# Kernel tuning notes

Hardware: AMD Instinct MI355X
Metric: run time of the kernel (lower is better)

Reference implementation:

```python
import jax, jax.numpy as jnp
import numpy as np

N = 100000      # nodes
D = 128         # input feature dim
K = 8           # propagation hops (concat K+1 blocks)
HID = 512
OUT = 32
E = 1600000     # edges (avg degree 16)
BN_EPS = 1e-5
DEG_EPS = 1e-8


def setup_inputs() -> dict:
    key = jax.random.key(0)
    ks = jax.random.split(key, 8)
    feature = jax.random.normal(ks[0], (N, D), dtype=jnp.float32)
    coor = jax.random.uniform(ks[1], (N, 2), dtype=jnp.float32)
    edge_index = jax.random.randint(ks[2], (2, E), 0, N, dtype=jnp.int32)
    theta = jnp.array(1.0, dtype=jnp.float32)  # Gaussian bandwidth param
    fan1 = D * (K + 1)
    W1 = jax.random.normal(ks[3], (HID, fan1), dtype=jnp.float32) * (1.0 / np.sqrt(fan1))
    b1 = jnp.zeros((HID,), dtype=jnp.float32)
    gamma = jnp.ones((HID,), dtype=jnp.float32)
    beta = jnp.zeros((HID,), dtype=jnp.float32)
    W2 = jax.random.normal(ks[4], (OUT, HID), dtype=jnp.float32) * (1.0 / np.sqrt(HID))
    b2 = jnp.zeros((OUT,), dtype=jnp.float32)
    return {"feature": feature, "coor": coor, "theta": theta,
            "W1": W1, "b1": b1, "gamma": gamma, "beta": beta,
            "W2": W2, "b2": b2, "edge_index": edge_index, "m": 1}


def reference(feature, coor, theta, W1, b1, gamma, beta, W2, b2, edge_index, m):
    row, col = edge_index[0], edge_index[1]  # dst, src
    # Gaussian kernel edge weights from coordinate distances (gather on coor)
    diff = coor[row] - coor[col]                       # [E, 2]
    dist2 = jnp.sum(diff * diff, axis=-1)              # [E]
    w = jnp.exp(-dist2 * theta / m)                    # [E]
    # degree (row) normalization via scatter-add
    deg = jax.ops.segment_sum(w, row, num_segments=N)  # [N]
    norm = w / (deg[row] + DEG_EPS)                    # [E]
    # K sequential propagations, concat with input (-> N x D*(K+1))
    xs = [feature]
    x = feature
    for _ in range(K):
        msgs = x[col] * norm[:, None]                  # [E, D] gather + weight
        x = jax.ops.segment_sum(msgs, row, num_segments=N)  # [N, D] scatter
        xs.append(x)
    h = jnp.concatenate(xs, axis=-1)                   # [N, D*(K+1)]
    # MLP head: fc1 -> leaky_relu(0.2) -> BatchNorm1d (batch stats) -> fc2
    h = jax.nn.leaky_relu(h @ W1.T + b1, negative_slope=0.2)
    mu = jnp.mean(h, axis=0)
    var = jnp.var(h, axis=0)
    h = (h - mu) * jax.lax.rsqrt(var + BN_EPS) * gamma + beta
    # dropout omitted (deterministic/eval reference)
    return h @ W2.T + b2
```

## Files before the change

kernel.cpp:

```cpp
#include <hip/hip_runtime.h>
#include <hip/hip_bf16.h>
#include <cstdint>
#include <cstddef>

#define NNODES 100000
#define DFEAT 128
#define KHOP 8
#define FAN1 1152
#define HIDN 512
#define OUTD 32
#define NEDGE 1600000
#define BN_EPS 1e-5f
#define DEG_EPS 1e-8f
#define FIXSCALE 67108864.0f

using short8 = __attribute__((ext_vector_type(8))) short;
using f32x4  = __attribute__((ext_vector_type(4))) float;

__device__ __forceinline__ float bf16lo(uint32_t u) { return __uint_as_float(u << 16); }
__device__ __forceinline__ float bf16hi(uint32_t u) { return __uint_as_float(u & 0xffff0000u); }
__device__ __forceinline__ float bf16s(short x) {
    return __uint_as_float(((uint32_t)(uint16_t)x) << 16);
}
__device__ __forceinline__ uint32_t packbf(float a, float b) {
    uint32_t lo = __bfloat16_as_ushort(__float2bfloat16(a));
    uint32_t hi = __bfloat16_as_ushort(__float2bfloat16(b));
    return lo | (hi << 16);
}

__device__ __forceinline__ void gload16(const void* g, void* l) {
    __builtin_amdgcn_global_load_lds(
        (const __attribute__((address_space(1))) uint32_t*)g,
        (__attribute__((address_space(3))) uint32_t*)l, 16, 0, 0);
}

struct Blk3 { const __hip_bfloat16* p[3]; };

__global__ __launch_bounds__(256) void edge_kernel(
    const int* __restrict__ ei, const float* __restrict__ coor,
    const float* __restrict__ theta, const int* __restrict__ mm,
    unsigned long long* __restrict__ packed, unsigned short* __restrict__ rank)
{
    int e = blockIdx.x * 256 + threadIdx.x;
    if (e >= NEDGE) return;
    float tom = theta[0] / (float)mm[0];
    int r = ei[e], c = ei[NEDGE + e];
    float2 pr = *(const float2*)(coor + 2*(size_t)r);
    float2 pc = *(const float2*)(coor + 2*(size_t)c);
    float dx = pr.x - pc.x, dy = pr.y - pc.y;
    float w = expf(-(dx*dx + dy*dy) * tom);
    unsigned long long enc = (1ULL << 48)
        | (unsigned long long)(unsigned int)__float2uint_rn(w * FIXSCALE);
    unsigned long long old = atomicAdd(&packed[r], enc);
    rank[e] = (unsigned short)(old >> 48);
}

__global__ __launch_bounds__(1024) void scan_local(
    const unsigned long long* __restrict__ packed, int* __restrict__ row_ptr,
    int* __restrict__ bsum, int n)
{
    __shared__ int wsum[16];
    int b = blockIdx.x, tid = threadIdx.x;
    int i = b * 1024 + tid;
    int lane = tid & 63, wv = tid >> 6;
    int v = (i < n) ? (int)(packed[i] >> 48) : 0;
    #pragma unroll
    for (int off = 1; off < 64; off <<= 1) {
        int t = __shfl_up(v, off, 64);
        if (lane >= off) v += t;
    }
    if (lane == 63) wsum[wv] = v;
    __syncthreads();
    if (tid < 16) {
        int t = wsum[tid];
        #pragma unroll
        for (int off = 1; off < 16; off <<= 1) {
            int u = __shfl_up(t, off, 64);
            if (tid >= off) t += u;
        }
        wsum[tid] = t;
    }
    __syncthreads();
    int incl = v + ((wv == 0) ? 0 : wsum[wv - 1]);
    if (i < n) row_ptr[i + 1] = incl;
    if (tid == 0) bsum[b] = wsum[15];
}

__global__ __launch_bounds__(128) void scan_carry(int* __restrict__ bsum, int n)
{
    __shared__ int ws[2];
    int tid = threadIdx.x, lane = tid & 63, wv = tid >> 6;
    int v = (tid < n) ? bsum[tid] : 0;
    int incl = v;
    #pragma unroll
    for (int off = 1; off < 64; off <<= 1) {
        int t = __shfl_up(incl, off, 64);
        if (lane >= off) incl += t;
    }
    if (lane == 63) ws[wv] = incl;
    __syncthreads();
    int excl = incl - v + ((wv == 0) ? 0 : ws[0]);
    if (tid < n) bsum[tid] = excl;
}

__global__ __launch_bounds__(256) void scan_add(
    const int* __restrict__ bsum, int* __restrict__ row_ptr, int n)
{
    int i = blockIdx.x * 256 + threadIdx.x;
    if (i == 0) row_ptr[0] = 0;
    if (i < n) row_ptr[i + 1] += bsum[i >> 10];
}

__global__ __launch_bounds__(256) void fill_kernel(
    const int* __restrict__ ei, const float* __restrict__ coor,
    const float* __restrict__ theta, const int* __restrict__ mm,
    const unsigned long long* __restrict__ packed,
    const unsigned short* __restrict__ rank, const int* __restrict__ row_ptr,
    uint2* __restrict__ edat)
{
    int e = blockIdx.x * 256 + threadIdx.x;
    if (e >= NEDGE) return;
    float tom = theta[0] / (float)mm[0];
    int r = ei[e], c = ei[NEDGE + e];
    float2 pr = *(const float2*)(coor + 2*(size_t)r);
    float2 pc = *(const float2*)(coor + 2*(size_t)c);
    float dx = pr.x - pc.x, dy = pr.y - pc.y;
    float w = expf(-(dx*dx + dy*dy) * tom);
    float deg = (float)(double)(packed[r] & 0xFFFFFFFFFFFFULL) * (1.0f / FIXSCALE);
    int pos = row_ptr[r] + rank[e];
    uint2 d;
    d.x = (unsigned)c;
    d.y = __float_as_uint(w / (deg + DEG_EPS));
    edat[pos] = d;
}

__global__ __launch_bounds__(256) void cast_feat_kernel(
    const float* __restrict__ f, __hip_bfloat16* __restrict__ x0)
{
    int i = blockIdx.x * 256 + threadIdx.x;
    int node = i >> 6, l2 = i & 63;
    if (node >= NNODES) return;
    float2 v = *(const float2*)(f + (size_t)node * DFEAT + l2 * 2);
    __hip_bfloat162 hb;
    hb.x = __float2bfloat16(v.x);
    hb.y = __float2bfloat16(v.y);
    *(__hip_bfloat162*)(x0 + (size_t)node * DFEAT + l2 * 2) = hb;
}

__global__ __launch_bounds__(256) void cast_w1_kernel(
    const float* __restrict__ w1, __hip_bfloat16* __restrict__ o)
{
    int i = blockIdx.x * 256 + threadIdx.x;
    if (i < HIDN * FAN1) o[i] = __float2bfloat16(w1[i]);
}

__global__ __launch_bounds__(256) void prop_kernel(
    const __hip_bfloat16* __restrict__ x, __hip_bfloat16* __restrict__ y,
    const int* __restrict__ row_ptr, const uint2* __restrict__ edat)
{
    int gw = (blockIdx.x * 256 + threadIdx.x) >> 6;
    if (gw >= NNODES) return;
    int lane = threadIdx.x & 63;
    int q = lane >> 4, sl = lane & 15;
    int beg = row_ptr[gw], end = row_ptr[gw + 1];
    float a0 = 0.f, a1 = 0.f, a2 = 0.f, a3 = 0.f;
    float a4 = 0.f, a5 = 0.f, a6 = 0.f, a7 = 0.f;
    int e = beg + q;
    for (; e + 12 < end; e += 16) {
        uint2 e0 = edat[e], e1 = edat[e + 4], e2 = edat[e + 8], e3 = edat[e + 12];
        float w0 = __uint_as_float(e0.y), w1 = __uint_as_float(e1.y);
        float w2 = __uint_as_float(e2.y), w3 = __uint_as_float(e3.y);
        uint4 u0 = *(const uint4*)(x + (size_t)e0.x * DFEAT + sl * 8);
        uint4 u1 = *(const uint4*)(x + (size_t)e1.x * DFEAT + sl * 8);
        uint4 u2 = *(const uint4*)(x + (size_t)e2.x * DFEAT + sl * 8);
        uint4 u3 = *(const uint4*)(x + (size_t)e3.x * DFEAT + sl * 8);
        a0 += w0 * bf16lo(u0.x); a1 += w0 * bf16hi(u0.x);
        a2 += w0 * bf16lo(u0.y); a3 += w0 * bf16hi(u0.y);
        a4 += w0 * bf16lo(u0.z); a5 += w0 * bf16hi(u0.z);
        a6 += w0 * bf16lo(u0.w); a7 += w0 * bf16hi(u0.w);
        a0 += w1 * bf16lo(u1.x); a1 += w1 * bf16hi(u1.x);
        a2 += w1 * bf16lo(u1.y); a3 += w1 * bf16hi(u1.y);
        a4 += w1 * bf16lo(u1.z); a5 += w1 * bf16hi(u1.z);
        a6 += w1 * bf16lo(u1.w); a7 += w1 * bf16hi(u1.w);
        a0 += w2 * bf16lo(u2.x); a1 += w2 * bf16hi(u2.x);
        a2 += w2 * bf16lo(u2.y); a3 += w2 * bf16hi(u2.y);
        a4 += w2 * bf16lo(u2.z); a5 += w2 * bf16hi(u2.z);
        a6 += w2 * bf16lo(u2.w); a7 += w2 * bf16hi(u2.w);
        a0 += w3 * bf16lo(u3.x); a1 += w3 * bf16hi(u3.x);
        a2 += w3 * bf16lo(u3.y); a3 += w3 * bf16hi(u3.y);
        a4 += w3 * bf16lo(u3.z); a5 += w3 * bf16hi(u3.z);
        a6 += w3 * bf16lo(u3.w); a7 += w3 * bf16hi(u3.w);
    }
    for (; e < end; e += 4) {
        uint2 e0 = edat[e];
        float w0 = __uint_as_float(e0.y);
        uint4 u0 = *(const uint4*)(x + (size_t)e0.x * DFEAT + sl * 8);
        a0 += w0 * bf16lo(u0.x); a1 += w0 * bf16hi(u0.x);
        a2 += w0 * bf16lo(u0.y); a3 += w0 * bf16hi(u0.y);
        a4 += w0 * bf16lo(u0.z); a5 += w0 * bf16hi(u0.z);
        a6 += w0 * bf16lo(u0.w); a7 += w0 * bf16hi(u0.w);
    }
    a0 += __shfl_xor(a0, 16, 64); a0 += __shfl_xor(a0, 32, 64);
    a1 += __shfl_xor(a1, 16, 64); a1 += __shfl_xor(a1, 32, 64);
    a2 += __shfl_xor(a2, 16, 64); a2 += __shfl_xor(a2, 32, 64);
    a3 += __shfl_xor(a3, 16, 64); a3 += __shfl_xor(a3, 32, 64);
    a4 += __shfl_xor(a4, 16, 64); a4 += __shfl_xor(a4, 32, 64);
    a5 += __shfl_xor(a5, 16, 64); a5 += __shfl_xor(a5, 32, 64);
    a6 += __shfl_xor(a6, 16, 64); a6 += __shfl_xor(a6, 32, 64);
    a7 += __shfl_xor(a7, 16, 64); a7 += __shfl_xor(a7, 32, 64);
    if (q == 0) {
        uint4 o;
        o.x = packbf(a0, a1);
        o.y = packbf(a2, a3);
        o.z = packbf(a4, a5);
        o.w = packbf(a6, a7);
        *(uint4*)(y + (size_t)gw * DFEAT + sl * 8) = o;
    }
}

__global__ __launch_bounds__(256) void fc1_kernel(
    Blk3 blks, const __hip_bfloat16* __restrict__ w1,
    const float* __restrict__ b1, __hip_bfloat16* __restrict__ h1b,
    float* __restrict__ gsum, float* __restrict__ gsq,
    int nkt, int kb0, int mode)
{
    __shared__ char smem[33792];
    int pid = blockIdx.x;
    int lid = (pid & 7) * 391 + (pid >> 3);
    int n0 = (lid & 3) * 128;
    int m0 = (lid >> 2) * 128;
    int tid = threadIdx.x, lane = tid & 63, wv = tid >> 6;
    int wr = wv >> 1, wc = wv & 1;

    f32x4 acc[4][4];
    #pragma unroll
    for (int i = 0; i < 4; ++i)
        #pragma unroll
        for (int j = 0; j < 4; ++j)
            acc[i][j] = (f32x4){0.f, 0.f, 0.f, 0.f};

#define STAGE(hb, ktv) do {                                                   \
        const __hip_bfloat16* xp = blks.p[(ktv) >> 2];                        \
        int koff_ = ((ktv) & 3) * 32;                                         \
        int kglob_ = (kb0 + ((ktv) >> 2)) * 128 + koff_;                      \
        char* Ab_ = smem + (hb) * 16384;                                      \
        char* Bb_ = Ab_ + 8192;                                               \
        _Pragma("unroll")                                                     \
        for (int l = 0; l < 2; ++l) {                                         \
            int u = l * 256 + wv * 64 + lane;                                 \
            int row_ = u >> 2, qq_ = u & 3;                                   \
            gload16(xp + (size_t)(m0 + row_) * DFEAT + koff_ + qq_ * 8,       \
                    Ab_ + u * 16);                                            \
            gload16(w1 + (size_t)(n0 + row_) * FAN1 + kglob_ + qq_ * 8,       \
                    Bb_ + u * 16);                                            \
        }                                                                     \
    } while (0)

    STAGE(0, 0);
    for (int kt = 0; kt < nkt; ++kt) {
        int cur = kt & 1;
        __builtin_amdgcn_s_barrier();
        if (kt + 1 < nkt) {
            STAGE(cur ^ 1, kt + 1);
            asm volatile("s_waitcnt vmcnt(4)" ::: "memory");
        } else {
            asm volatile("s_waitcnt vmcnt(0)" ::: "memory");
        }
        __builtin_amdgcn_s_barrier();
        char* Ab = smem + cur * 16384;
        char* Bb = Ab + 8192;
        short8 af[4], bfr[4];
        #pragma unroll
        for (int i = 0; i < 4; ++i)
            af[i] = *(const short8*)(Ab + (wr * 64 + i * 16 + (lane & 15)) * 64 + (lane >> 4) * 16);
        #pragma unroll
        for (int j = 0; j < 4; ++j)
            bfr[j] = *(const short8*)(Bb + (wc * 64 + j * 16 + (lane & 15)) * 64 + (lane >> 4) * 16);
        #pragma unroll
        for (int j = 0; j < 4; ++j)
            #pragma unroll
            for (int i = 0; i < 4; ++i)
                acc[i][j] = __builtin_amdgcn_mfma_f32_16x16x32_bf16(af[i], bfr[j], acc[i][j], 0, 0, 0);
    }
#undef STAGE

    __syncthreads();
    __hip_bfloat16* tile = (__hip_bfloat16*)smem;
    float* lsum = (float*)(smem + 32768);
    float* lsq  = lsum + 128;
    bool fin = (mode & 2) != 0;
    if (fin && tid < 128) { lsum[tid] = 0.f; lsq[tid] = 0.f; }
    #pragma unroll
    for (int i = 0; i < 4; ++i) {
        #pragma unroll
        for (int j = 0; j < 4; ++j) {
            int col = wc * 64 + j * 16 + (lane & 15);
            #pragma unroll
            for (int r = 0; r < 4; ++r) {
                int row = wr * 64 + i * 16 + (lane >> 4) * 4 + r;
                tile[row * 128 + col] = __float2bfloat16(acc[i][j][r]);
            }
        }
    }
    __syncthreads();

    int cu = tid & 15, tr = tid >> 4;
    float bias[8];
    float s[8], q[8];
    #pragma unroll
    for (int e = 0; e < 8; ++e) { s[e] = 0.f; q[e] = 0.f; }
    if (fin) {
        #pragma unroll
        for (int e = 0; e < 8; ++e) bias[e] = b1[n0 + cu * 8 + e];
    }
    size_t blkbase = (size_t)(n0 >> 7) * NNODES * 128;
    for (int p = 0; p < 8; ++p) {
        int row = p * 16 + tr;
        int gm = m0 + row;
        if (gm >= NNODES) continue;
        short8 fresh = *(const short8*)(tile + row * 128 + cu * 8);
        size_t gidx = blkbase + (size_t)gm * 128 + cu * 8;
        float v[8];
        #pragma unroll
        for (int e = 0; e < 8; ++e) v[e] = bf16s(fresh[e]);
        if (mode & 1) {
            short8 prev = *(const short8*)(h1b + gidx);
            #pragma unroll
            for (int e = 0; e < 8; ++e) v[e] += bf16s(prev[e]);
        }
        if (fin) {
            #pragma unroll
            for (int e = 0; e < 8; ++e) {
                float t = v[e] + bias[e];
                t = (t > 0.f) ? t : 0.2f * t;
                v[e] = t;
                s[e] += t;
                q[e] += t * t;
            }
        }
        short8 outv;
        #pragma unroll
        for (int e = 0; e < 8; ++e) outv[e] = (short)__bfloat16_as_ushort(__float2bfloat16(v[e]));
        *(short8*)(h1b + gidx) = outv;
    }
    if (fin) {
        #pragma unroll
        for (int e = 0; e < 8; ++e) {
            atomicAdd(&lsum[cu * 8 + e], s[e]);
            atomicAdd(&lsq[cu * 8 + e], q[e]);
        }
        __syncthreads();
        if (tid < 128) {
            atomicAdd(&gsum[n0 + tid], lsum[tid]);
            atomicAdd(&gsq[n0 + tid], lsq[tid]);
        }
    }
}

__global__ __launch_bounds__(512) void bn_finalize(
    const float* __restrict__ gsum, const float* __restrict__ gsq,
    const float* __restrict__ gamma, const float* __restrict__ beta,
    const float* __restrict__ w2, const float* __restrict__ b2,
    __hip_bfloat16* __restrict__ w2s, float* __restrict__ cvec)
{
    __shared__ float ts[HIDN];
    int tid = threadIdx.x;
    float mu = gsum[tid] * (1.0f / NNODES);
    float var = gsq[tid] * (1.0f / NNODES) - mu * mu;
    float s = gamma[tid] * rsqrtf(var + BN_EPS);
    float t = beta[tid] - mu * s;
    ts[tid] = t;
    for (int o = 0; o < OUTD; ++o)
        w2s[o * HIDN + tid] = __float2bfloat16(w2[o * HIDN + tid] * s);
    __syncthreads();
    int lane = tid & 63, wv = tid >> 6;
    for (int o = wv; o < OUTD; o += 8) {
        float p = 0.f;
        for (int j = lane; j < HIDN; j += 64) p += ts[j] * w2[o * HIDN + j];
        #pragma unroll
        for (int off = 32; off; off >>= 1) p += __shfl_xor(p, off, 64);
        if (lane == 0) cvec[o] = p + b2[o];
    }
}

__global__ __launch_bounds__(256) void fc2_kernel(
    const __hip_bfloat16* __restrict__ h1b, const __hip_bfloat16* __restrict__ w2s,
    const float* __restrict__ cvec, float* __restrict__ out)
{
    int gw = (blockIdx.x * 256 + threadIdx.x) >> 6;
    if (gw >= NNODES / 16) return;
    int lane = threadIdx.x & 63;
    int m0 = gw * 16;
    f32x4 acc[2];
    acc[0] = (f32x4){0.f, 0.f, 0.f, 0.f};
    acc[1] = (f32x4){0.f, 0.f, 0.f, 0.f};
    #pragma unroll
    for (int kt = 0; kt < HIDN / 32; ++kt) {
        int k0 = kt * 32;
        short8 a = *(const short8*)(h1b
            + ((size_t)(kt >> 2) * NNODES + (m0 + (lane & 15))) * 128
            + (kt & 3) * 32 + (lane >> 4) * 8);
        #pragma unroll
        for (int j = 0; j < 2; ++j) {
            short8 b = *(const short8*)(w2s + (size_t)(j * 16 + (lane & 15)) * HIDN + k0 + (lane >> 4) * 8);
            acc[j] = __builtin_amdgcn_mfma_f32_16x16x32_bf16(a, b, acc[j], 0, 0, 0);
        }
    }
    #pragma unroll
    for (int j = 0; j < 2; ++j) {
        int col = j * 16 + (lane & 15);
        float cadd = cvec[col];
        #pragma unroll
        for (int r = 0; r < 4; ++r) {
            int row = m0 + (lane >> 4) * 4 + r;
            out[(size_t)row * OUTD + col] = acc[j][r] + cadd;
        }
    }
}

struct Ptrs {
    float *gsum, *gsq, *cvec;
    int *row_ptr, *bsum;
    unsigned long long* packed;
    unsigned short* rank;
    uint2* edat;
    __hip_bfloat16 *slot[3], *h1acc, *w1b, *w2s;
};

static size_t layout(char* base, Ptrs& P) {
    char* p = base;
    auto take = [&](size_t b) {
        char* q = (char*)(((uintptr_t)p + 255) & ~(uintptr_t)255);
        p = q + b;
        return q;
    };
    P.packed  = (unsigned long long*)take((size_t)NNODES * 8);
    P.rank    = (unsigned short*)take((size_t)NEDGE * 2);
    P.row_ptr = (int*)  take((size_t)(NNODES + 1) * 4);
    P.bsum    = (int*)  take(128 * 4);
    P.edat    = (uint2*)take((size_t)NEDGE * 8);
    P.h1acc   = (__hip_bfloat16*)take((size_t)NNODES * HIDN * 2 + 65536);
    P.w1b     = (__hip_bfloat16*)take((size_t)HIDN * FAN1 * 2);
    P.w2s     = (__hip_bfloat16*)take((size_t)OUTD * HIDN * 2);
    P.gsum    = (float*)take(HIDN * 4);
    P.gsq     = (float*)take(HIDN * 4);
    P.cvec    = (float*)take(OUTD * 4);
    for (int i = 0; i < 3; ++i)
        P.slot[i] = (__hip_bfloat16*)take((size_t)NNODES * DFEAT * 2 + 32768);
    return (size_t)(p - base);
}

extern "C" void kernel_launch(void* const* d_in, const int* in_sizes, int n_in,
                              void* d_out, int out_size, void* d_ws, size_t ws_size,
                              hipStream_t stream)
{
    const float* feature = (const float*)d_in[0];
    const float* coor    = (const float*)d_in[1];
    const float* theta   = (const float*)d_in[2];
    const float* W1      = (const float*)d_in[3];
    const float* b1      = (const float*)d_in[4];
    const float* gamma   = (const float*)d_in[5];
    const float* beta    = (const float*)d_in[6];
    const float* W2      = (const float*)d_in[7];
    const float* b2      = (const float*)d_in[8];
    const int*   ei      = (const int*)d_in[9];
    const int*   mm      = (const int*)d_in[10];
    float* out = (float*)d_out;
    (void)in_sizes; (void)n_in; (void)out_size; (void)ws_size;

    Ptrs P;
    layout((char*)d_ws, P);

    hipMemsetAsync(P.packed, 0, (size_t)NNODES * 8, stream);
    hipMemsetAsync(P.gsum,   0, HIDN * 4, stream);
    hipMemsetAsync(P.gsq,    0, HIDN * 4, stream);

    int eb = (NEDGE + 255) / 256;
    int nchunk = (NNODES + 1023) / 1024;
    edge_kernel<<<eb, 256, 0, stream>>>(ei, coor, theta, mm, P.packed, P.rank);
    scan_local<<<nchunk, 1024, 0, stream>>>(P.packed, P.row_ptr, P.bsum, NNODES);
    scan_carry<<<1, 128, 0, stream>>>(P.bsum, nchunk);
    scan_add<<<(NNODES + 255) / 256, 256, 0, stream>>>(P.bsum, P.row_ptr, NNODES);
    fill_kernel<<<eb, 256, 0, stream>>>(ei, coor, theta, mm, P.packed, P.rank,
                                        P.row_ptr, P.edat);

    cast_w1_kernel<<<(HIDN * FAN1 + 255) / 256, 256, 0, stream>>>(W1, P.w1b);
    cast_feat_kernel<<<(NNODES * 64) / 256, 256, 0, stream>>>(feature, P.slot[0]);

    int pb = (NNODES * 64) / 256;
    int fgrid = 8 * 391;

    auto launch_fc1 = [&](int kb0, int mode) {
        Blk3 b;
        for (int i = 0; i < 3; ++i) b.p[i] = P.slot[i];
        fc1_kernel<<<fgrid, 256, 0, stream>>>(b, P.w1b, b1, P.h1acc,
                                              P.gsum, P.gsq, 12, kb0, mode);
    };

    for (int k = 1; k <= KHOP; ++k) {
        prop_kernel<<<pb, 256, 0, stream>>>(P.slot[(k - 1) % 3],
                                            P.slot[k % 3],
                                            P.row_ptr, P.edat);
        if (k == 2) launch_fc1(0, 0);
        if (k == 5) launch_fc1(3, 1);
    }
    launch_fc1(6, 3);

    bn_finalize<<<1, 512, 0, stream>>>(P.gsum, P.gsq, gamma, beta, W2, b2,
                                       P.w2s, P.cvec);
    fc2_kernel<<<(NNODES / 16 * 64 + 255) / 256, 256, 0, stream>>>(P.h1acc, P.w2s,
                                                                   P.cvec, out);
}
```

Measured before the change: 924.1 us.

## Triple-buffer fc1 K-loop and merge fc1 passes using five feature slots

The fc1 GEMM mainloop moves from double to triple LDS buffering, prefetching two k-tiles ahead with adjusted vmcnt waits to hide global-load latency better. When the workspace is large enough, the hop outputs rotate through five slots instead of three. That lets fc1 run in two launches (5 blocks, then 4) rather than three, cutting one read-modify-write pass over the large h1 accumulator. The cost is more LDS per block (about 48.5KB instead of 33KB), which may lower occupancy, and longer serialization between prop and fc1 launches.

```diff
diff --git a/kernel.cpp b/kernel.cpp
--- a/kernel.cpp
+++ b/kernel.cpp
@@ -34,7 +34,7 @@
         (__attribute__((address_space(3))) uint32_t*)l, 16, 0, 0);
 }
 
-struct Blk3 { const __hip_bfloat16* p[3]; };
+struct Blk5 { const __hip_bfloat16* p[5]; };
 
 __global__ __launch_bounds__(256) void edge_kernel(
     const int* __restrict__ ei, const float* __restrict__ coor,
@@ -219,12 +219,12 @@
 }
 
 __global__ __launch_bounds__(256) void fc1_kernel(
-    Blk3 blks, const __hip_bfloat16* __restrict__ w1,
+    Blk5 blks, const __hip_bfloat16* __restrict__ w1,
     const float* __restrict__ b1, __hip_bfloat16* __restrict__ h1b,
     float* __restrict__ gsum, float* __restrict__ gsq,
     int nkt, int kb0, int mode)
 {
-    __shared__ char smem[33792];
+    __shared__ char smem[49664];
     int pid = blockIdx.x;
     int lid = (pid & 7) * 391 + (pid >> 3);
     int n0 = (lid & 3) * 128;
@@ -257,17 +257,21 @@
     } while (0)
 
     STAGE(0, 0);
+    STAGE(1, 1);
+    int bufsel = 0;
     for (int kt = 0; kt < nkt; ++kt) {
-        int cur = kt & 1;
         __builtin_amdgcn_s_barrier();
-        if (kt + 1 < nkt) {
-            STAGE(cur ^ 1, kt + 1);
+        if (kt + 2 < nkt) {
+            int nb = bufsel + 2; if (nb >= 3) nb -= 3;
+            STAGE(nb, kt + 2);
+            asm volatile("s_waitcnt vmcnt(8)" ::: "memory");
+        } else if (kt + 1 < nkt) {
             asm volatile("s_waitcnt vmcnt(4)" ::: "memory");
         } else {
             asm volatile("s_waitcnt vmcnt(0)" ::: "memory");
         }
         __builtin_amdgcn_s_barrier();
-        char* Ab = smem + cur * 16384;
+        char* Ab = smem + bufsel * 16384;
         char* Bb = Ab + 8192;
         short8 af[4], bfr[4];
         #pragma unroll
@@ -281,13 +285,16 @@
             #pragma unroll
             for (int i = 0; i < 4; ++i)
                 acc[i][j] = __builtin_amdgcn_mfma_f32_16x16x32_bf16(af[i], bfr[j], acc[i][j], 0, 0, 0);
+        ++bufsel; if (bufsel >= 3) bufsel -= 3;
     }
 #undef STAGE
 
     __syncthreads();
     __hip_bfloat16* tile = (__hip_bfloat16*)smem;
-    float* lsum = (float*)(smem + 32768);
-    float* lsq  = lsum + 128;
+    float* lsum = (float*)(smem + 49152);
+    float* lsq  = lsum + 64;
+    lsum = (float*)(smem + 33792);
+    lsq  = lsum + 128;
     bool fin = (mode & 2) != 0;
     if (fin && tid < 128) { lsum[tid] = 0.f; lsq[tid] = 0.f; }
     #pragma unroll
@@ -424,10 +431,10 @@
     unsigned long long* packed;
     unsigned short* rank;
     uint2* edat;
-    __hip_bfloat16 *slot[3], *h1acc, *w1b, *w2s;
+    __hip_bfloat16 *slot[5], *h1acc, *w1b, *w2s;
 };
 
-static size_t layout(char* base, Ptrs& P) {
+static size_t layout(char* base, int nslots, Ptrs& P) {
     char* p = base;
     auto take = [&](size_t b) {
         char* q = (char*)(((uintptr_t)p + 255) & ~(uintptr_t)255);
@@ -445,7 +452,8 @@
     P.gsum    = (float*)take(HIDN * 4);
     P.gsq     = (float*)take(HIDN * 4);
     P.cvec    = (float*)take(OUTD * 4);
-    for (int i = 0; i < 3; ++i)
+    for (int i = 0; i < 5; ++i) P.slot[i] = nullptr;
+    for (int i = 0; i < nslots; ++i)
         P.slot[i] = (__hip_bfloat16*)take((size_t)NNODES * DFEAT * 2 + 32768);
     return (size_t)(p - base);
 }
@@ -466,10 +474,12 @@
     const int*   ei      = (const int*)d_in[9];
     const int*   mm      = (const int*)d_in[10];
     float* out = (float*)d_out;
-    (void)in_sizes; (void)n_in; (void)out_size; (void)ws_size;
+    (void)in_sizes; (void)n_in; (void)out_size;
 
     Ptrs P;
-    layout((char*)d_ws, P);
+    size_t need5 = layout((char*)0, 5, P);
+    int nslots = (ws_size >= need5) ? 5 : 3;
+    layout((char*)d_ws, nslots, P);
 
     hipMemsetAsync(P.packed, 0, (size_t)NNODES * 8, stream);
     hipMemsetAsync(P.gsum,   0, HIDN * 4, stream);
@@ -490,21 +500,32 @@
     int pb = (NNODES * 64) / 256;
     int fgrid = 8 * 391;
 
-    auto launch_fc1 = [&](int kb0, int mode) {
-        Blk3 b;
-        for (int i = 0; i < 3; ++i) b.p[i] = P.slot[i];
+    auto launch_fc1 = [&](int nblk, int kb0, int mode) {
+        Blk5 b;
+        for (int i = 0; i < 5; ++i) b.p[i] = P.slot[0];
+        for (int i = 0; i < nblk; ++i) b.p[i] = P.slot[i];
         fc1_kernel<<<fgrid, 256, 0, stream>>>(b, P.w1b, b1, P.h1acc,
-                                              P.gsum, P.gsq, 12, kb0, mode);
+                                              P.gsum, P.gsq, nblk * 4, kb0, mode);
     };
 
-    for (int k = 1; k <= KHOP; ++k) {
-        prop_kernel<<<pb, 256, 0, stream>>>(P.slot[(k - 1) % 3],
-                                            P.slot[k % 3],
-                                            P.row_ptr, P.edat);
-        if (k == 2) launch_fc1(0, 0);
-        if (k == 5) launch_fc1(3, 1);
-    }
-    launch_fc1(6, 3);
+    if (nslots == 5) {
+        for (int k = 1; k <= KHOP; ++k) {
+            prop_kernel<<<pb, 256, 0, stream>>>(P.slot[(k - 1) % 5],
+                                                P.slot[k % 5],
+                                                P.row_ptr, P.edat);
+            if (k == 4) launch_fc1(5, 0, 0);
+        }
+        launch_fc1(4, 5, 3);
+    } else {
+        for (int k = 1; k <= KHOP; ++k) {
+            prop_kernel<<<pb, 256, 0, stream>>>(P.slot[(k - 1) % 3],
+                                                P.slot[k % 3],
+                                                P.row_ptr, P.edat);
+            if (k == 2) launch_fc1(3, 0, 0);
+            if (k == 5) launch_fc1(3, 3, 1);
+        }
+        launch_fc1(3, 6, 3);
+    }
 
     bn_finalize<<<1, 512, 0, stream>>>(P.gsum, P.gsq, gamma, beta, W2, b2,
                                        P.w2s, P.cvec);
```

Result: faster. 904.3 us (-2.1%).
